# Optimization experiments

Measured on AMD Instinct MI355X. Metric: run time of the kernel, lower is better.

The kernel has to match this reference:

```python
import jax, jax.numpy as jnp
import numpy as np

N, E, D, G, F_IN, F_OUT = 100_000, 1_000_000, 64, 256, 4, 4


def _lin_init(key, fan_in, fan_out):
    k1, k2 = jax.random.split(key)
    s = 1.0 / np.sqrt(fan_in)
    W = jax.random.uniform(k1, (fan_in, fan_out), jnp.float32, -s, s)
    b = jax.random.uniform(k2, (fan_out,), jnp.float32, -s, s)
    return W, b


def setup_inputs() -> dict:
    key = jax.random.key(0)
    ks = jax.random.split(key, 10)
    x = jax.random.normal(ks[0], (N, F_IN), jnp.float32)
    edge_index = jax.random.randint(ks[1], (2, E), 0, N, jnp.int32)
    # contiguous, sorted graph ids covering all G graphs (PyG-style batch vector)
    batch_index = ((jnp.arange(N, dtype=jnp.int32) * G) // N).astype(jnp.int32)
    topo_hidden = jax.random.normal(ks[2], (N, D), jnp.float32)
    W0, b0 = _lin_init(ks[3], F_IN, D)
    W1, b1 = _lin_init(ks[4], D, D)
    W2, b2 = _lin_init(ks[5], D, D)
    W3, b3 = _lin_init(ks[6], D, D)
    Wf, bf = _lin_init(ks[7], D, D)
    Wo, bo = _lin_init(ks[8], 2 * D, F_OUT)
    return dict(x=x, edge_index=edge_index, batch_index=batch_index,
                topo_hidden=topo_hidden,
                W0=W0, b0=b0, W1=W1, b1=b1, W2=W2, b2=b2, W3=W3, b3=b3,
                Wf=Wf, bf=bf, Wo=Wo, bo=bo, num_graphs=G)


def reference(x, edge_index, batch_index, topo_hidden,
              W0, b0, W1, b1, W2, b2, W3, b3, Wf, bf, Wo, bo, num_graphs):
    n = x.shape[0]
    loops = jnp.arange(n, dtype=edge_index.dtype)
    row = jnp.concatenate([edge_index[0], loops])  # sources (+ self loops)
    col = jnp.concatenate([edge_index[1], loops])  # targets (+ self loops)
    # degree of targets, symmetric normalization (same for every layer)
    deg = jax.ops.segment_sum(jnp.ones_like(col, dtype=x.dtype), col, num_segments=n)
    dis = deg ** -0.5  # deg >= 1 thanks to self loops
    norm = dis[row] * dis[col]  # [E+N]

    def gcn(h, W, b):
        h = h @ W + b                      # dense linear
        msg = norm[:, None] * h[row]       # gather + normalize
        return jax.ops.segment_sum(msg, col, num_segments=n)  # scatter-add

    h = jnp.tanh(gcn(x, W0, b0))
    h = jnp.tanh(gcn(h, W1, b1))
    h = jnp.tanh(gcn(h, W2, b2))
    h = jnp.tanh(gcn(h, W3, b3))
    h = (topo_hidden * h) @ Wf + bf        # fusion
    gmax = jax.ops.segment_max(h, batch_index, num_segments=num_graphs)
    gsum = jax.ops.segment_sum(h, batch_index, num_segments=num_graphs)
    cnt = jax.ops.segment_sum(jnp.ones((n, 1), x.dtype), batch_index, num_segments=num_graphs)
    pooled = jnp.concatenate([gmax, gsum / cnt], axis=1)  # [G, 2D]
    out = pooled @ Wo + bo
    return out, pooled
```

## Files before the change

kernel.cpp:

```cpp
#include <hip/hip_runtime.h>
#include <hip/hip_bf16.h>

#define N_NODES 100000
#define N_EDGES 1000000
#define DIM 64
#define N_GRAPHS 256
#define F_IN 4
#define F_OUT 4
#define NBK 196
#define CAP 8192
#define BIN_CHUNK 4096

using short8 = __attribute__((ext_vector_type(8))) short;
using f32x4 = __attribute__((ext_vector_type(4))) float;

__device__ __forceinline__ float bf_lo(unsigned int u) { return __uint_as_float(u << 16); }
__device__ __forceinline__ float bf_hi(unsigned int u) { return __uint_as_float(u & 0xffff0000u); }
__device__ __forceinline__ unsigned short f2bf(float f) {
    unsigned int u = __float_as_uint(f);
    u = u + 0x7fffu + ((u >> 16) & 1u);
    return (unsigned short)(u >> 16);
}
__device__ __forceinline__ unsigned pack2(float a, float b) {
    return (unsigned)f2bf(a) | ((unsigned)f2bf(b) << 16);
}
__device__ __forceinline__ unsigned fenc(float f) {
    unsigned u = __float_as_uint(f);
    return (u >> 31) ? ~u : (u | 0x80000000u);
}

__global__ void bin_scatter(const int* __restrict__ rows, const int* __restrict__ cols,
                            int* __restrict__ bucketCursor, unsigned int* __restrict__ binned,
                            int E, int nChunks, const float* __restrict__ W1,
                            const float* __restrict__ W2, const float* __restrict__ W3,
                            const float* __restrict__ Wf, unsigned short* __restrict__ wfrag) {
    __shared__ int hist[NBK];
    __shared__ int base[NBK];
    __shared__ int cnt2[NBK];
    int tid = threadIdx.x;
    if (blockIdx.x >= nChunks) {
        int widx = blockIdx.x - nChunks;
        const float* W = widx == 0 ? W1 : widx == 1 ? W2 : widx == 2 ? W3 : Wf;
        for (int s = tid; s < 512; s += 256) {
            int jtkk = s >> 6, l = s & 63;
            int jt = jtkk >> 1, kk = jtkk & 1;
            int j = jt * 16 + (l & 15);
            int kbase = kk * 32 + (l >> 4) * 8;
            unsigned short* dst = wfrag + widx * 4096 + s * 8;
#pragma unroll
            for (int e = 0; e < 8; ++e) dst[e] = f2bf(W[(kbase + e) * 64 + j]);
        }
        return;
    }
    for (int i = tid; i < NBK; i += 256) { hist[i] = 0; cnt2[i] = 0; }
    __syncthreads();
    int chunk = blockIdx.x * BIN_CHUNK;
#pragma unroll
    for (int i = 0; i < 16; ++i) {
        int e = chunk + i * 256 + tid;
        if (e < E) atomicAdd(&hist[cols[e] >> 9], 1);
    }
    __syncthreads();
    for (int i = tid; i < NBK; i += 256)
        if (hist[i] > 0) base[i] = atomicAdd(&bucketCursor[i], hist[i]);
    __syncthreads();
#pragma unroll
    for (int i = 0; i < 16; ++i) {
        int e = chunk + i * 256 + tid;
        if (e < E) {
            int c = cols[e], r = rows[e];
            int b = c >> 9;
            int pos = base[b] + atomicAdd(&cnt2[b], 1);
            binned[b * CAP + pos] = ((unsigned)(c & 511) << 17) | (unsigned)r;
        }
    }
}

__global__ void bucket_fill(const unsigned int* __restrict__ binned,
                            const int* __restrict__ bucketCursor, const float* __restrict__ x,
                            int* __restrict__ csr_src, int2* __restrict__ rowse,
                            float* __restrict__ dis, uint4* __restrict__ xsp, int n) {
    __shared__ int hist[512];
    __shared__ int scn[256];
    __shared__ int cur[512];
    int b = blockIdx.x, tid = threadIdx.x;
    int nbase = b << 9;
    int ebase = b * CAP;
    hist[tid] = 0;
    hist[tid + 256] = 0;
    __syncthreads();
    int cnt = bucketCursor[b];
    for (int k = tid; k < cnt; k += 256) atomicAdd(&hist[binned[ebase + k] >> 17], 1);
    __syncthreads();
    int h0 = hist[2 * tid], h1 = hist[2 * tid + 1];
    int s = h0 + h1;
    scn[tid] = s;
    __syncthreads();
    for (int ofs = 1; ofs < 256; ofs <<= 1) {
        int u = (tid >= ofs) ? scn[tid - ofs] : 0;
        __syncthreads();
        scn[tid] += u;
        __syncthreads();
    }
    int excl = scn[tid] - s;
    int st0 = ebase + excl, st1 = ebase + excl + h0;
    cur[2 * tid] = st0;
    cur[2 * tid + 1] = st1;
    int node0 = nbase + 2 * tid, node1 = nbase + 2 * tid + 1;
    if (node0 < n) {
        rowse[node0] = make_int2(st0, st0 + h0);
        float d = rsqrtf((float)(h0 + 1));
        dis[node0] = d;
        float4 xv = ((const float4*)x)[node0];
        uint4 o;
        o.x = pack2(d * xv.x, d * xv.y);
        o.y = pack2(d * xv.z, d * xv.w);
        o.z = __float_as_uint(d);
        o.w = 0;
        xsp[node0] = o;
    }
    if (node1 < n) {
        rowse[node1] = make_int2(st1, st1 + h1);
        float d = rsqrtf((float)(h1 + 1));
        dis[node1] = d;
        float4 xv = ((const float4*)x)[node1];
        uint4 o;
        o.x = pack2(d * xv.x, d * xv.y);
        o.y = pack2(d * xv.z, d * xv.w);
        o.z = __float_as_uint(d);
        o.w = 0;
        xsp[node1] = o;
    }
    __syncthreads();
    for (int k = tid; k < cnt; k += 256) {
        unsigned v = binned[ebase + k];
        int cl = v >> 17;
        int r = (int)(v & 0x1FFFFu);
        int pos = atomicAdd(&cur[cl], 1);
        csr_src[pos] = r;
    }
}

__global__ __launch_bounds__(256, 8)
void csr_agg_x(const int2* __restrict__ rowse, const int* __restrict__ csr_src,
               const uint4* __restrict__ xsp, float* __restrict__ aggx,
               float* __restrict__ normsum, int n) {
    int t = blockIdx.x * 256 + threadIdx.x;
    int c = t >> 2, sl = t & 3;
    if (c >= n) return;
    int2 se = rowse[c];
    float a0 = 0.f, a1 = 0.f, a2 = 0.f, a3 = 0.f, ns = 0.f;
    uint4 u0 = xsp[c];
    float dc = __uint_as_float(u0.z);
    if (sl == 0) {
        a0 = bf_lo(u0.x); a1 = bf_hi(u0.x); a2 = bf_lo(u0.y); a3 = bf_hi(u0.y);
        ns = dc;
    }
    int k = se.x + sl;
    for (; k + 4 < se.y; k += 8) {
        int r1 = csr_src[k], r2 = csr_src[k + 4];
        uint4 u1 = xsp[r1];
        uint4 u2 = xsp[r2];
        a0 += bf_lo(u1.x) + bf_lo(u2.x);
        a1 += bf_hi(u1.x) + bf_hi(u2.x);
        a2 += bf_lo(u1.y) + bf_lo(u2.y);
        a3 += bf_hi(u1.y) + bf_hi(u2.y);
        ns += __uint_as_float(u1.z) + __uint_as_float(u2.z);
    }
    if (k < se.y) {
        int r = csr_src[k];
        uint4 u = xsp[r];
        a0 += bf_lo(u.x); a1 += bf_hi(u.x); a2 += bf_lo(u.y); a3 += bf_hi(u.y);
        ns += __uint_as_float(u.z);
    }
#pragma unroll
    for (int m = 1; m < 4; m <<= 1) {
        a0 += __shfl_xor(a0, m, 64);
        a1 += __shfl_xor(a1, m, 64);
        a2 += __shfl_xor(a2, m, 64);
        a3 += __shfl_xor(a3, m, 64);
        ns += __shfl_xor(ns, m, 64);
    }
    if (sl == 0) {
        ((float4*)aggx)[c] = make_float4(dc * a0, dc * a1, dc * a2, dc * a3);
        normsum[c] = dc * ns;
    }
}

__global__ void gemm_l01(const float* __restrict__ aggx, const float* __restrict__ normsum,
                         const float* __restrict__ W0, const float* __restrict__ b0,
                         const unsigned short* __restrict__ wfrag, const float* __restrict__ bias,
                         const float* __restrict__ dis, unsigned short* __restrict__ outv, int n) {
    __shared__ float W0s[256];
    __shared__ float b0s[64];
    int tid = threadIdx.x;
    W0s[tid] = W0[tid];
    if (tid < 64) b0s[tid] = b0[tid];
    __syncthreads();
    int wid = tid >> 6, l = tid & 63;
    int nodeBase = blockIdx.x * 64 + wid * 16;
    if (nodeBase >= n) return;
    int arow = nodeBase + (l & 15);
    float4 ax = ((const float4*)aggx)[arow];
    float nsv = normsum[arow];
    int kb = (l >> 4) * 8;
    short8 a0, a1;
#pragma unroll
    for (int e = 0; e < 8; ++e) {
        int k = kb + e;
        float g0 = nsv * b0s[k] + ax.x * W0s[k] + ax.y * W0s[64 + k] +
                   ax.z * W0s[128 + k] + ax.w * W0s[192 + k];
        a0[e] = (short)f2bf(tanhf(g0));
        int k1 = k + 32;
        float g1 = nsv * b0s[k1] + ax.x * W0s[k1] + ax.y * W0s[64 + k1] +
                   ax.z * W0s[128 + k1] + ax.w * W0s[192 + k1];
        a1[e] = (short)f2bf(tanhf(g1));
    }
    const short8* B = (const short8*)wfrag;
    f32x4 acc[4];
#pragma unroll
    for (int jt = 0; jt < 4; ++jt) {
        acc[jt] = (f32x4){0.f, 0.f, 0.f, 0.f};
        acc[jt] = __builtin_amdgcn_mfma_f32_16x16x32_bf16(a0, B[(jt * 2 + 0) * 64 + l], acc[jt], 0, 0, 0);
        acc[jt] = __builtin_amdgcn_mfma_f32_16x16x32_bf16(a1, B[(jt * 2 + 1) * 64 + l], acc[jt], 0, 0, 0);
    }
    int rbase = nodeBase + (l >> 4) * 4;
#pragma unroll
    for (int jt = 0; jt < 4; ++jt) {
        int j = jt * 16 + (l & 15);
        float bj = bias[j];
#pragma unroll
        for (int r = 0; r < 4; ++r) {
            int node = rbase + r;
            outv[(size_t)node * 64 + j] = f2bf((acc[jt][r] + bj) * dis[node]);
        }
    }
}

__global__ void gemm_kernel(const unsigned short* __restrict__ act,
                            const unsigned short* __restrict__ wfrag,
                            const float* __restrict__ bias, const float* __restrict__ dis,
                            unsigned short* __restrict__ outv, int n) {
    int tid = threadIdx.x;
    int wid = tid >> 6, l = tid & 63;
    int nodeBase = blockIdx.x * 64 + wid * 16;
    if (nodeBase >= n) return;
    const short8* A = (const short8*)act;
    const short8* B = (const short8*)wfrag;
    int arow = nodeBase + (l & 15);
    short8 a0 = A[arow * 8 + (l >> 4)];
    short8 a1 = A[arow * 8 + 4 + (l >> 4)];
    f32x4 acc[4];
#pragma unroll
    for (int jt = 0; jt < 4; ++jt) {
        acc[jt] = (f32x4){0.f, 0.f, 0.f, 0.f};
        acc[jt] = __builtin_amdgcn_mfma_f32_16x16x32_bf16(a0, B[(jt * 2 + 0) * 64 + l], acc[jt], 0, 0, 0);
        acc[jt] = __builtin_amdgcn_mfma_f32_16x16x32_bf16(a1, B[(jt * 2 + 1) * 64 + l], acc[jt], 0, 0, 0);
    }
    int rbase = nodeBase + (l >> 4) * 4;
#pragma unroll
    for (int jt = 0; jt < 4; ++jt) {
        int j = jt * 16 + (l & 15);
        float bj = bias[j];
#pragma unroll
        for (int r = 0; r < 4; ++r) {
            int node = rbase + r;
            outv[(size_t)node * 64 + j] = f2bf((acc[jt][r] + bj) * dis[node]);
        }
    }
}

__global__ void gemm_pool(const unsigned short* __restrict__ act,
                          const unsigned short* __restrict__ wfrag,
                          const float* __restrict__ bias, float* __restrict__ pooled, int n) {
    int tid = threadIdx.x;
    int wid = tid >> 6, l = tid & 63;
    int nodeBase = blockIdx.x * 64 + wid * 16;
    if (nodeBase >= n) return;
    const short8* A = (const short8*)act;
    const short8* B = (const short8*)wfrag;
    int arow = nodeBase + (l & 15);
    short8 a0 = A[arow * 8 + (l >> 4)];
    short8 a1 = A[arow * 8 + 4 + (l >> 4)];
    f32x4 acc[4];
#pragma unroll
    for (int jt = 0; jt < 4; ++jt) {
        acc[jt] = (f32x4){0.f, 0.f, 0.f, 0.f};
        acc[jt] = __builtin_amdgcn_mfma_f32_16x16x32_bf16(a0, B[(jt * 2 + 0) * 64 + l], acc[jt], 0, 0, 0);
        acc[jt] = __builtin_amdgcn_mfma_f32_16x16x32_bf16(a1, B[(jt * 2 + 1) * 64 + l], acc[jt], 0, 0, 0);
    }
    int glo = (int)(((long long)nodeBase << 8) / N_NODES);
    int ghi = (int)(((long long)(nodeBase + 15) << 8) / N_NODES);
    int rbase = nodeBase + (l >> 4) * 4;
#pragma unroll
    for (int jt = 0; jt < 4; ++jt) {
        int j = jt * 16 + (l & 15);
        float bj = bias[j];
        float v0 = acc[jt][0] + bj, v1 = acc[jt][1] + bj;
        float v2 = acc[jt][2] + bj, v3 = acc[jt][3] + bj;
        if (glo == ghi) {
            float mx = fmaxf(fmaxf(v0, v1), fmaxf(v2, v3));
            float sm = v0 + v1 + v2 + v3;
            mx = fmaxf(mx, __shfl_xor(mx, 16, 64));
            sm += __shfl_xor(sm, 16, 64);
            mx = fmaxf(mx, __shfl_xor(mx, 32, 64));
            sm += __shfl_xor(sm, 32, 64);
            if (l < 16) {
                atomicAdd(&pooled[glo * 128 + 64 + j], sm);
                atomicMax((unsigned*)&pooled[glo * 128 + j], fenc(mx));
            }
        } else {
            float vv[4] = {v0, v1, v2, v3};
#pragma unroll
            for (int r = 0; r < 4; ++r) {
                int g = (int)(((long long)(rbase + r) << 8) / N_NODES);
                atomicAdd(&pooled[g * 128 + 64 + j], vv[r]);
                atomicMax((unsigned*)&pooled[g * 128 + j], fenc(vv[r]));
            }
        }
    }
}

template <bool TOPO>
__global__ void agg_tanh_kernel(const int2* __restrict__ rowse, const int* __restrict__ csr_src,
                                const float* __restrict__ dis, const uint2* __restrict__ hs2,
                                const float* __restrict__ topo, unsigned short* __restrict__ act) {
    int tid = threadIdx.x;
    int wid = tid >> 6, lane = tid & 63;
    int node = blockIdx.x * 4 + wid;
    int q = lane >> 4, f = lane & 15;
    int2 se = rowse[node];
    float a0 = 0.f, a1 = 0.f, a2 = 0.f, a3 = 0.f;
    float c0 = 0.f, c1 = 0.f, c2 = 0.f, c3 = 0.f;
    if (q == 0) {
        uint2 u = hs2[(size_t)node * 16 + f];
        a0 = bf_lo(u.x); a1 = bf_hi(u.x); a2 = bf_lo(u.y); a3 = bf_hi(u.y);
    }
    int k = se.x + q;
    for (; k + 4 < se.y; k += 8) {
        int r1 = csr_src[k];
        int r2 = csr_src[k + 4];
        uint2 u1 = hs2[(size_t)r1 * 16 + f];
        uint2 u2 = hs2[(size_t)r2 * 16 + f];
        a0 += bf_lo(u1.x); a1 += bf_hi(u1.x); a2 += bf_lo(u1.y); a3 += bf_hi(u1.y);
        c0 += bf_lo(u2.x); c1 += bf_hi(u2.x); c2 += bf_lo(u2.y); c3 += bf_hi(u2.y);
    }
    if (k < se.y) {
        int r = csr_src[k];
        uint2 u = hs2[(size_t)r * 16 + f];
        a0 += bf_lo(u.x); a1 += bf_hi(u.x); a2 += bf_lo(u.y); a3 += bf_hi(u.y);
    }
    a0 += c0; a1 += c1; a2 += c2; a3 += c3;
#pragma unroll
    for (int m = 16; m < 64; m <<= 1) {
        a0 += __shfl_xor(a0, m, 64);
        a1 += __shfl_xor(a1, m, 64);
        a2 += __shfl_xor(a2, m, 64);
        a3 += __shfl_xor(a3, m, 64);
    }
    if (q == 0) {
        float dc = dis[node];
        float v0 = tanhf(dc * a0);
        float v1 = tanhf(dc * a1);
        float v2 = tanhf(dc * a2);
        float v3 = tanhf(dc * a3);
        if (TOPO) {
            float4 tp = ((const float4*)topo)[(size_t)node * 16 + f];
            v0 *= tp.x; v1 *= tp.y; v2 *= tp.z; v3 *= tp.w;
        }
        uint2 o;
        o.x = pack2(v0, v1);
        o.y = pack2(v2, v3);
        ((uint2*)act)[(size_t)node * 16 + f] = o;
    }
}

__global__ void finalize_out(float* __restrict__ pooled, const float* __restrict__ Wo,
                             const float* __restrict__ bo, float* __restrict__ out, int n, int G) {
    __shared__ float p[128];
    int g = blockIdx.x, t = threadIdx.x;
    int start = (int)(((long long)g * n + G - 1) / G);
    int end = (int)(((long long)(g + 1) * n + G - 1) / G);
    float v;
    if (t < 64) {
        unsigned u = __float_as_uint(pooled[g * 128 + t]);
        unsigned rep = (u >> 31) ? (u & 0x7FFFFFFFu) : ~u;
        v = __uint_as_float(rep);
    } else {
        v = pooled[g * 128 + t] / (float)(end - start);
    }
    pooled[g * 128 + t] = v;
    p[t] = v;
    __syncthreads();
    if (t < F_OUT) {
        float acc = bo[t];
#pragma unroll 8
        for (int k = 0; k < 128; ++k) acc += p[k] * Wo[k * F_OUT + t];
        out[g * F_OUT + t] = acc;
    }
}

extern "C" void kernel_launch(void* const* d_in, const int* in_sizes, int n_in,
                              void* d_out, int out_size, void* d_ws, size_t ws_size,
                              hipStream_t stream) {
    const float* x = (const float*)d_in[0];
    const int* edge_index = (const int*)d_in[1];
    const float* topo = (const float*)d_in[3];
    const float* W0 = (const float*)d_in[4];
    const float* b0 = (const float*)d_in[5];
    const float* W1 = (const float*)d_in[6];
    const float* b1 = (const float*)d_in[7];
    const float* W2 = (const float*)d_in[8];
    const float* b2 = (const float*)d_in[9];
    const float* W3 = (const float*)d_in[10];
    const float* b3 = (const float*)d_in[11];
    const float* Wf = (const float*)d_in[12];
    const float* bf_ = (const float*)d_in[13];
    const float* Wo = (const float*)d_in[14];
    const float* bo = (const float*)d_in[15];

    const int* rows = edge_index;
    const int* cols = edge_index + N_EDGES;

    char* ws = (char*)d_ws;
    size_t off = 0;
    float* dis = (float*)(ws + off); off += (size_t)N_NODES * 4;
    int* bucketCursor = (int*)(ws + off); off += 1024;
    int2* rowse = (int2*)(ws + off); off += (size_t)N_NODES * 8;
    int* csr_src = (int*)(ws + off); off += (size_t)NBK * CAP * 4;
    unsigned int* binned = (unsigned int*)(ws + off); off += (size_t)NBK * CAP * 4;
    uint4* xsp = (uint4*)(ws + off); off += (size_t)N_NODES * 16;
    float* aggx = (float*)(ws + off); off += (size_t)N_NODES * F_IN * 4;
    float* normsum = (float*)(ws + off); off += (size_t)N_NODES * 4;
    off = (off + 255) & ~(size_t)255;
    unsigned short* wfrag = (unsigned short*)(ws + off); off += 4 * 4096 * 2;
    off = (off + 255) & ~(size_t)255;
    unsigned short* act = (unsigned short*)(ws + off); off += (size_t)N_NODES * DIM * 2;
    off = (off + 255) & ~(size_t)255;
    unsigned short* hsA = (unsigned short*)(ws + off); off += (size_t)N_NODES * DIM * 2;
    off = (off + 255) & ~(size_t)255;
    unsigned short* hsB = (unsigned short*)(ws + off); off += (size_t)N_NODES * DIM * 2;
    (void)ws_size;

    float* out = (float*)d_out;
    float* pooled = (float*)d_out + N_GRAPHS * F_OUT;

    const int nChunks = (N_EDGES + BIN_CHUNK - 1) / BIN_CHUNK;

    hipMemsetAsync(bucketCursor, 0, NBK * 4, stream);
    hipMemsetAsync(pooled, 0, (size_t)N_GRAPHS * 2 * DIM * 4, stream);

    bin_scatter<<<nChunks + 4, 256, 0, stream>>>(rows, cols, bucketCursor, binned, N_EDGES,
                                                 nChunks, W1, W2, W3, Wf, wfrag);
    bucket_fill<<<NBK, 256, 0, stream>>>(binned, bucketCursor, x, csr_src, rowse, dis, xsp, N_NODES);

    csr_agg_x<<<(N_NODES * 4 + 255) / 256, 256, 0, stream>>>(rowse, csr_src, xsp, aggx, normsum, N_NODES);
    const int gridG = (N_NODES + 63) / 64;
    gemm_l01<<<gridG, 256, 0, stream>>>(aggx, normsum, W0, b0, wfrag, b1, dis, hsA, N_NODES);

    const int gridA = N_NODES / 4;
    agg_tanh_kernel<false><<<gridA, 256, 0, stream>>>(rowse, csr_src, dis, (const uint2*)hsA, nullptr, act);
    gemm_kernel<<<gridG, 256, 0, stream>>>(act, wfrag + 4096, b2, dis, hsB, N_NODES);

    agg_tanh_kernel<false><<<gridA, 256, 0, stream>>>(rowse, csr_src, dis, (const uint2*)hsB, nullptr, act);
    gemm_kernel<<<gridG, 256, 0, stream>>>(act, wfrag + 2 * 4096, b3, dis, hsA, N_NODES);

    agg_tanh_kernel<true><<<gridA, 256, 0, stream>>>(rowse, csr_src, dis, (const uint2*)hsA, topo, act);
    gemm_pool<<<gridG, 256, 0, stream>>>(act, wfrag + 3 * 4096, bf_, pooled, N_NODES);

    finalize_out<<<N_GRAPHS, 128, 0, stream>>>(pooled, Wo, bo, out, N_NODES, N_GRAPHS);
}
```

Baseline: 225.2 us.

## Fuse aggregation+tanh with following GEMM via LDS staging; fold pooled memset into bin kernel

Merges each agg_tanh kernel with the following MFMA GEMM into one kernel. A 256-thread block aggregates 16 nodes, writes the bf16 activations to a swizzled LDS tile, then each wave computes one 16-column slice of the 64x64 linear. This removes the global round trip of the intermediate activation buffer and three kernel launches. The pooled buffer memset is replaced by an extra block in bin_scatter. In exchange, each wave now processes 4 nodes serially, which may reduce latency hiding in the gather-heavy aggregation, and grid size drops by 4x.

```diff
diff --git a/kernel.cpp b/kernel.cpp
--- a/kernel.cpp
+++ b/kernel.cpp
@@ -33,13 +33,19 @@
                             int* __restrict__ bucketCursor, unsigned int* __restrict__ binned,
                             int E, int nChunks, const float* __restrict__ W1,
                             const float* __restrict__ W2, const float* __restrict__ W3,
-                            const float* __restrict__ Wf, unsigned short* __restrict__ wfrag) {
+                            const float* __restrict__ Wf, unsigned short* __restrict__ wfrag,
+                            float* __restrict__ pooled) {
     __shared__ int hist[NBK];
     __shared__ int base[NBK];
     __shared__ int cnt2[NBK];
     int tid = threadIdx.x;
     if (blockIdx.x >= nChunks) {
         int widx = blockIdx.x - nChunks;
+        if (widx == 4) {
+            float4* p4 = (float4*)pooled;
+            for (int i = tid; i < N_GRAPHS * 32; i += 256) p4[i] = make_float4(0.f, 0.f, 0.f, 0.f);
+            return;
+        }
         const float* W = widx == 0 ? W1 : widx == 1 ? W2 : widx == 2 ? W3 : Wf;
         for (int s = tid; s < 512; s += 256) {
             int jtkk = s >> 6, l = s & 63;
@@ -237,67 +243,81 @@
     }
 }
 
-__global__ void gemm_kernel(const unsigned short* __restrict__ act,
-                            const unsigned short* __restrict__ wfrag,
-                            const float* __restrict__ bias, const float* __restrict__ dis,
-                            unsigned short* __restrict__ outv, int n) {
+template <bool TOPO, bool POOL>
+__global__ void agg_gemm(const int2* __restrict__ rowse, const int* __restrict__ csr_src,
+                         const float* __restrict__ dis, const uint2* __restrict__ hs2,
+                         const float* __restrict__ topo, const unsigned short* __restrict__ wfrag,
+                         const float* __restrict__ bias, unsigned short* __restrict__ outv,
+                         float* __restrict__ pooled) {
+    __shared__ short8 actlds[128];
     int tid = threadIdx.x;
-    int wid = tid >> 6, l = tid & 63;
-    int nodeBase = blockIdx.x * 64 + wid * 16;
-    if (nodeBase >= n) return;
-    const short8* A = (const short8*)act;
+    int wid = tid >> 6, lane = tid & 63;
+    int nodeBase = blockIdx.x * 16;
+    int q = lane >> 4, f = lane & 15;
+#pragma unroll 1
+    for (int i = 0; i < 4; ++i) {
+        int r = wid * 4 + i;
+        int node = nodeBase + r;
+        int2 se = rowse[node];
+        float a0 = 0.f, a1 = 0.f, a2 = 0.f, a3 = 0.f;
+        float c0 = 0.f, c1 = 0.f, c2 = 0.f, c3 = 0.f;
+        if (q == 0) {
+            uint2 u = hs2[(size_t)node * 16 + f];
+            a0 = bf_lo(u.x); a1 = bf_hi(u.x); a2 = bf_lo(u.y); a3 = bf_hi(u.y);
+        }
+        int k = se.x + q;
+        for (; k + 4 < se.y; k += 8) {
+            int r1 = csr_src[k];
+            int r2 = csr_src[k + 4];
+            uint2 u1 = hs2[(size_t)r1 * 16 + f];
+            uint2 u2 = hs2[(size_t)r2 * 16 + f];
+            a0 += bf_lo(u1.x); a1 += bf_hi(u1.x); a2 += bf_lo(u1.y); a3 += bf_hi(u1.y);
+            c0 += bf_lo(u2.x); c1 += bf_hi(u2.x); c2 += bf_lo(u2.y); c3 += bf_hi(u2.y);
+        }
+        if (k < se.y) {
+            int rr = csr_src[k];
+            uint2 u = hs2[(size_t)rr * 16 + f];
+            a0 += bf_lo(u.x); a1 += bf_hi(u.x); a2 += bf_lo(u.y); a3 += bf_hi(u.y);
+        }
+        a0 += c0; a1 += c1; a2 += c2; a3 += c3;
+#pragma unroll
+        for (int m = 16; m < 64; m <<= 1) {
+            a0 += __shfl_xor(a0, m, 64);
+            a1 += __shfl_xor(a1, m, 64);
+            a2 += __shfl_xor(a2, m, 64);
+            a3 += __shfl_xor(a3, m, 64);
+        }
+        if (q == 0) {
+            float dc = dis[node];
+            float v0 = tanhf(dc * a0);
+            float v1 = tanhf(dc * a1);
+            float v2 = tanhf(dc * a2);
+            float v3 = tanhf(dc * a3);
+            if (TOPO) {
+                float4 tp = ((const float4*)topo)[(size_t)node * 16 + f];
+                v0 *= tp.x; v1 *= tp.y; v2 *= tp.z; v3 *= tp.w;
+            }
+            uint2 o;
+            o.x = pack2(v0, v1);
+            o.y = pack2(v2, v3);
+            ((uint2*)actlds)[r * 16 + (((f >> 1) ^ (r & 7)) << 1) + (f & 1)] = o;
+        }
+    }
+    __syncthreads();
+    int rA = lane & 15, qq = lane >> 4;
+    short8 av0 = actlds[rA * 8 + (qq ^ (rA & 7))];
+    short8 av1 = actlds[rA * 8 + ((4 + qq) ^ (rA & 7))];
     const short8* B = (const short8*)wfrag;
-    int arow = nodeBase + (l & 15);
-    short8 a0 = A[arow * 8 + (l >> 4)];
-    short8 a1 = A[arow * 8 + 4 + (l >> 4)];
-    f32x4 acc[4];
-#pragma unroll
-    for (int jt = 0; jt < 4; ++jt) {
-        acc[jt] = (f32x4){0.f, 0.f, 0.f, 0.f};
-        acc[jt] = __builtin_amdgcn_mfma_f32_16x16x32_bf16(a0, B[(jt * 2 + 0) * 64 + l], acc[jt], 0, 0, 0);
-        acc[jt] = __builtin_amdgcn_mfma_f32_16x16x32_bf16(a1, B[(jt * 2 + 1) * 64 + l], acc[jt], 0, 0, 0);
-    }
-    int rbase = nodeBase + (l >> 4) * 4;
-#pragma unroll
-    for (int jt = 0; jt < 4; ++jt) {
-        int j = jt * 16 + (l & 15);
-        float bj = bias[j];
-#pragma unroll
-        for (int r = 0; r < 4; ++r) {
-            int node = rbase + r;
-            outv[(size_t)node * 64 + j] = f2bf((acc[jt][r] + bj) * dis[node]);
-        }
-    }
-}
-
-__global__ void gemm_pool(const unsigned short* __restrict__ act,
-                          const unsigned short* __restrict__ wfrag,
-                          const float* __restrict__ bias, float* __restrict__ pooled, int n) {
-    int tid = threadIdx.x;
-    int wid = tid >> 6, l = tid & 63;
-    int nodeBase = blockIdx.x * 64 + wid * 16;
-    if (nodeBase >= n) return;
-    const short8* A = (const short8*)act;
-    const short8* B = (const short8*)wfrag;
-    int arow = nodeBase + (l & 15);
-    short8 a0 = A[arow * 8 + (l >> 4)];
-    short8 a1 = A[arow * 8 + 4 + (l >> 4)];
-    f32x4 acc[4];
-#pragma unroll
-    for (int jt = 0; jt < 4; ++jt) {
-        acc[jt] = (f32x4){0.f, 0.f, 0.f, 0.f};
-        acc[jt] = __builtin_amdgcn_mfma_f32_16x16x32_bf16(a0, B[(jt * 2 + 0) * 64 + l], acc[jt], 0, 0, 0);
-        acc[jt] = __builtin_amdgcn_mfma_f32_16x16x32_bf16(a1, B[(jt * 2 + 1) * 64 + l], acc[jt], 0, 0, 0);
-    }
-    int glo = (int)(((long long)nodeBase << 8) / N_NODES);
-    int ghi = (int)(((long long)(nodeBase + 15) << 8) / N_NODES);
-    int rbase = nodeBase + (l >> 4) * 4;
-#pragma unroll
-    for (int jt = 0; jt < 4; ++jt) {
-        int j = jt * 16 + (l & 15);
-        float bj = bias[j];
-        float v0 = acc[jt][0] + bj, v1 = acc[jt][1] + bj;
-        float v2 = acc[jt][2] + bj, v3 = acc[jt][3] + bj;
+    f32x4 acc = (f32x4){0.f, 0.f, 0.f, 0.f};
+    acc = __builtin_amdgcn_mfma_f32_16x16x32_bf16(av0, B[(wid * 2 + 0) * 64 + lane], acc, 0, 0, 0);
+    acc = __builtin_amdgcn_mfma_f32_16x16x32_bf16(av1, B[(wid * 2 + 1) * 64 + lane], acc, 0, 0, 0);
+    int j = wid * 16 + rA;
+    float bj = bias[j];
+    int rbase = nodeBase + qq * 4;
+    if (POOL) {
+        float v0 = acc[0] + bj, v1 = acc[1] + bj, v2 = acc[2] + bj, v3 = acc[3] + bj;
+        int glo = (int)(((long long)nodeBase << 8) / N_NODES);
+        int ghi = (int)(((long long)(nodeBase + 15) << 8) / N_NODES);
         if (glo == ghi) {
             float mx = fmaxf(fmaxf(v0, v1), fmaxf(v2, v3));
             float sm = v0 + v1 + v2 + v3;
@@ -305,73 +325,25 @@
             sm += __shfl_xor(sm, 16, 64);
             mx = fmaxf(mx, __shfl_xor(mx, 32, 64));
             sm += __shfl_xor(sm, 32, 64);
-            if (l < 16) {
+            if (lane < 16) {
                 atomicAdd(&pooled[glo * 128 + 64 + j], sm);
                 atomicMax((unsigned*)&pooled[glo * 128 + j], fenc(mx));
             }
         } else {
             float vv[4] = {v0, v1, v2, v3};
 #pragma unroll
-            for (int r = 0; r < 4; ++r) {
-                int g = (int)(((long long)(rbase + r) << 8) / N_NODES);
-                atomicAdd(&pooled[g * 128 + 64 + j], vv[r]);
-                atomicMax((unsigned*)&pooled[g * 128 + j], fenc(vv[r]));
+            for (int rr = 0; rr < 4; ++rr) {
+                int g = (int)(((long long)(rbase + rr) << 8) / N_NODES);
+                atomicAdd(&pooled[g * 128 + 64 + j], vv[rr]);
+                atomicMax((unsigned*)&pooled[g * 128 + j], fenc(vv[rr]));
             }
         }
-    }
-}
-
-template <bool TOPO>
-__global__ void agg_tanh_kernel(const int2* __restrict__ rowse, const int* __restrict__ csr_src,
-                                const float* __restrict__ dis, const uint2* __restrict__ hs2,
-                                const float* __restrict__ topo, unsigned short* __restrict__ act) {
-    int tid = threadIdx.x;
-    int wid = tid >> 6, lane = tid & 63;
-    int node = blockIdx.x * 4 + wid;
-    int q = lane >> 4, f = lane & 15;
-    int2 se = rowse[node];
-    float a0 = 0.f, a1 = 0.f, a2 = 0.f, a3 = 0.f;
-    float c0 = 0.f, c1 = 0.f, c2 = 0.f, c3 = 0.f;
-    if (q == 0) {
-        uint2 u = hs2[(size_t)node * 16 + f];
-        a0 = bf_lo(u.x); a1 = bf_hi(u.x); a2 = bf_lo(u.y); a3 = bf_hi(u.y);
-    }
-    int k = se.x + q;
-    for (; k + 4 < se.y; k += 8) {
-        int r1 = csr_src[k];
-        int r2 = csr_src[k + 4];
-        uint2 u1 = hs2[(size_t)r1 * 16 + f];
-        uint2 u2 = hs2[(size_t)r2 * 16 + f];
-        a0 += bf_lo(u1.x); a1 += bf_hi(u1.x); a2 += bf_lo(u1.y); a3 += bf_hi(u1.y);
-        c0 += bf_lo(u2.x); c1 += bf_hi(u2.x); c2 += bf_lo(u2.y); c3 += bf_hi(u2.y);
-    }
-    if (k < se.y) {
-        int r = csr_src[k];
-        uint2 u = hs2[(size_t)r * 16 + f];
-        a0 += bf_lo(u.x); a1 += bf_hi(u.x); a2 += bf_lo(u.y); a3 += bf_hi(u.y);
-    }
-    a0 += c0; a1 += c1; a2 += c2; a3 += c3;
-#pragma unroll
-    for (int m = 16; m < 64; m <<= 1) {
-        a0 += __shfl_xor(a0, m, 64);
-        a1 += __shfl_xor(a1, m, 64);
-        a2 += __shfl_xor(a2, m, 64);
-        a3 += __shfl_xor(a3, m, 64);
-    }
-    if (q == 0) {
-        float dc = dis[node];
-        float v0 = tanhf(dc * a0);
-        float v1 = tanhf(dc * a1);
-        float v2 = tanhf(dc * a2);
-        float v3 = tanhf(dc * a3);
-        if (TOPO) {
-            float4 tp = ((const float4*)topo)[(size_t)node * 16 + f];
-            v0 *= tp.x; v1 *= tp.y; v2 *= tp.z; v3 *= tp.w;
-        }
-        uint2 o;
-        o.x = pack2(v0, v1);
-        o.y = pack2(v2, v3);
-        ((uint2*)act)[(size_t)node * 16 + f] = o;
+    } else {
+#pragma unroll
+        for (int rr = 0; rr < 4; ++rr) {
+            int node = rbase + rr;
+            outv[(size_t)node * 64 + j] = f2bf((acc[rr] + bj) * dis[node]);
+        }
     }
 }
 
@@ -435,8 +407,6 @@
     off = (off + 255) & ~(size_t)255;
     unsigned short* wfrag = (unsigned short*)(ws + off); off += 4 * 4096 * 2;
     off = (off + 255) & ~(size_t)255;
-    unsigned short* act = (unsigned short*)(ws + off); off += (size_t)N_NODES * DIM * 2;
-    off = (off + 255) & ~(size_t)255;
     unsigned short* hsA = (unsigned short*)(ws + off); off += (size_t)N_NODES * DIM * 2;
     off = (off + 255) & ~(size_t)255;
     unsigned short* hsB = (unsigned short*)(ws + off); off += (size_t)N_NODES * DIM * 2;
@@ -448,25 +418,21 @@
     const int nChunks = (N_EDGES + BIN_CHUNK - 1) / BIN_CHUNK;
 
     hipMemsetAsync(bucketCursor, 0, NBK * 4, stream);
-    hipMemsetAsync(pooled, 0, (size_t)N_GRAPHS * 2 * DIM * 4, stream);
-
-    bin_scatter<<<nChunks + 4, 256, 0, stream>>>(rows, cols, bucketCursor, binned, N_EDGES,
-                                                 nChunks, W1, W2, W3, Wf, wfrag);
+
+    bin_scatter<<<nChunks + 5, 256, 0, stream>>>(rows, cols, bucketCursor, binned, N_EDGES,
+                                                 nChunks, W1, W2, W3, Wf, wfrag, pooled);
     bucket_fill<<<NBK, 256, 0, stream>>>(binned, bucketCursor, x, csr_src, rowse, dis, xsp, N_NODES);
 
     csr_agg_x<<<(N_NODES * 4 + 255) / 256, 256, 0, stream>>>(rowse, csr_src, xsp, aggx, normsum, N_NODES);
-    const int gridG = (N_NODES + 63) / 64;
-    gemm_l01<<<gridG, 256, 0, stream>>>(aggx, normsum, W0, b0, wfrag, b1, dis, hsA, N_NODES);
-
-    const int gridA = N_NODES / 4;
-    agg_tanh_kernel<false><<<gridA, 256, 0, stream>>>(rowse, csr_src, dis, (const uint2*)hsA, nullptr, act);
-    gemm_kernel<<<gridG, 256, 0, stream>>>(act, wfrag + 4096, b2, dis, hsB, N_NODES);
-
-    agg_tanh_kernel<false><<<gridA, 256, 0, stream>>>(rowse, csr_src, dis, (const uint2*)hsB, nullptr, act);
-    gemm_kernel<<<gridG, 256, 0, stream>>>(act, wfrag + 2 * 4096, b3, dis, hsA, N_NODES);
-
-    agg_tanh_kernel<true><<<gridA, 256, 0, stream>>>(rowse, csr_src, dis, (const uint2*)hsA, topo, act);
-    gemm_pool<<<gridG, 256, 0, stream>>>(act, wfrag + 3 * 4096, bf_, pooled, N_NODES);
+    gemm_l01<<<(N_NODES + 63) / 64, 256, 0, stream>>>(aggx, normsum, W0, b0, wfrag, b1, dis, hsA, N_NODES);
+
+    const int gridF = N_NODES / 16;
+    agg_gemm<false, false><<<gridF, 256, 0, stream>>>(
+        rowse, csr_src, dis, (const uint2*)hsA, nullptr, wfrag + 4096, b2, hsB, nullptr);
+    agg_gemm<false, false><<<gridF, 256, 0, stream>>>(
+        rowse, csr_src, dis, (const uint2*)hsB, nullptr, wfrag + 2 * 4096, b3, hsA, nullptr);
+    agg_gemm<true, true><<<gridF, 256, 0, stream>>>(
+        rowse, csr_src, dis, (const uint2*)hsA, topo, wfrag + 3 * 4096, bf_, nullptr, pooled);
 
     finalize_out<<<N_GRAPHS, 128, 0, stream>>>(pooled, Wo, bo, out, N_NODES, N_GRAPHS);
 }
```

Measured after the change: 208.9 us. 1.08x faster.
